# Kernel tuning notes

Hardware: AMD Instinct MI355X
Metric: run time of the kernel (lower is better)

Reference implementation:

```python
import jax, jax.numpy as jnp
import numpy as np

B = 65536      # batch
C = 1000       # num_classes
D = 256        # feat_dim


def _l2norm(x, eps=1e-12):
    # matches F.normalize(dim=1): v / max(||v||_2, eps)
    n = jnp.linalg.norm(x, axis=1, keepdims=True)
    return x / jnp.maximum(n, eps)


def setup_inputs() -> dict:
    key = jax.random.key(0)
    k1, k2, k3, k4, k5 = jax.random.split(key, 5)
    bound = 1.0 / np.sqrt(D)
    X = jax.random.normal(k1, (B, D), dtype=jnp.float32)
    labels = jax.random.randint(k2, (B,), 0, C)
    signatures = jax.random.uniform(k3, (C, D), dtype=jnp.float32, minval=-bound, maxval=bound)
    b_means = jax.random.uniform(k4, (1, D), dtype=jnp.float32, minval=-bound, maxval=bound)
    b_covs = jax.random.normal(k5, (D, D), dtype=jnp.float32)
    return {"X": X, "labels": labels, "signatures": signatures,
            "b_means": b_means, "b_covs": b_covs}


def reference(X, labels, signatures, b_means, b_covs):
    # SVD-based whitening of background covariance (tiny DxD)
    cov = b_covs @ b_covs.T
    U, eig, _ = jnp.linalg.svd(cov)
    DU = (eig ** -0.5)[:, None] * U.T              # diag(eig^-1/2) @ U^T, [D, D]
    xHat = _l2norm((X - b_means) @ DU.T)           # [B, D]
    sHat = _l2norm(signatures @ DU.T)              # [C, D]
    ACE_targets = xHat @ sHat.T                    # [B, C] cosine scores
    labels = labels.astype(jnp.int32)
    numerator = jnp.take_along_axis(ACE_targets, labels[:, None], axis=1)[:, 0]
    # denominator = exp(true) + sum(exp(others)) == sum over all classes
    loss = -jnp.mean(numerator - jax.nn.logsumexp(ACE_targets, axis=1))
    return (loss, ACE_targets)
```

## Files before the change

### kernel.cpp

```cpp
#include <hip/hip_runtime.h>
#include <hip/hip_bf16.h>
#include <math.h>

#define D_ 256
#define B_ 65536
#define C_ 1000

typedef _Float16 f16x8 __attribute__((ext_vector_type(8)));
typedef _Float16 f16x4 __attribute__((ext_vector_type(4)));
typedef float f32x4 __attribute__((ext_vector_type(4)));

__global__ void transpose_kernel(const float* __restrict__ in, float* __restrict__ out,
                                 double* __restrict__ acc) {
  __shared__ float t[32][33];
  if (blockIdx.x == 0 && threadIdx.x == 0) *acc = 0.0;
  const int bx = blockIdx.x & 7, by = blockIdx.x >> 3;
  const int lx = threadIdx.x & 31, ly = threadIdx.x >> 5;
#pragma unroll
  for (int s = 0; s < 4; ++s) {
    int r = by * 32 + ly + s * 8;
    t[ly + s * 8][lx] = in[r * 256 + bx * 32 + lx];
  }
  __syncthreads();
#pragma unroll
  for (int s = 0; s < 4; ++s) {
    int r = bx * 32 + ly + s * 8;
    out[r * 256 + by * 32 + lx] = t[lx][ly + s * 8];
  }
}

__global__ void cov_kernel(const float* __restrict__ bc, const float* __restrict__ bcT,
                           double* __restrict__ C64) {
  const int i = blockIdx.x, j = threadIdx.x;
  __shared__ float ri[D_];
  ri[j] = bc[i * D_ + j];
  __syncthreads();
  double s = 0.0;
#pragma unroll 8
  for (int k = 0; k < D_; ++k) s += (double)ri[k] * (double)bcT[k * D_ + j];
  C64[i * D_ + j] = s;
}

__global__ __launch_bounds__(256, 1) void chol_panel(double* __restrict__ A, int p) {
  const int j0 = p * 64;
  const int r = threadIdx.x;
  __shared__ double rowv[64];
  __shared__ double dinv;
  double pr[64];
  const bool act = (r >= j0);
  if (act) {
#pragma unroll
    for (int k = 0; k < 64; ++k) pr[k] = A[(size_t)r * D_ + j0 + k];
  }
#pragma unroll
  for (int j = 0; j < 64; ++j) {
    const int col = j0 + j;
    if (r == col) { double d = sqrt(pr[j]); pr[j] = d; dinv = 1.0 / d; }
    __syncthreads();
    if (r > col) {
      double lr = pr[j] * dinv;
      pr[j] = lr;
      if (r < j0 + 64) rowv[r - j0] = lr;
    }
    __syncthreads();
    if (r > col) {
      const double lr = pr[j];
#pragma unroll
      for (int k = j + 1; k < 64; ++k) pr[k] -= lr * rowv[k];
    }
  }
  if (act) {
    const int kmax = (r - j0 < 63) ? (r - j0) : 63;
#pragma unroll
    for (int k = 0; k < 64; ++k)
      if (k <= kmax) A[(size_t)r * D_ + j0 + k] = pr[k];
  }
}

__global__ __launch_bounds__(256) void chol_trail(double* __restrict__ A, int p) {
  const int j0 = p * 64;
  const int t0 = j0 + 64;
  int b = blockIdx.x, I = 0;
  while (b >= I + 1) { b -= I + 1; ++I; }
  const int J = b;
  const int r0 = t0 + I * 64, c0 = t0 + J * 64;
  __shared__ double LR[64][67];
  __shared__ double LC[64][67];
  const int tid = threadIdx.x;
  for (int e = tid; e < 64 * 64; e += 256) {
    int rr = e >> 6, cc = e & 63;
    LR[rr][cc] = A[(size_t)(r0 + rr) * D_ + j0 + cc];
    LC[rr][cc] = A[(size_t)(c0 + rr) * D_ + j0 + cc];
  }
  __syncthreads();
  const int tx = tid & 15, ty = tid >> 4;
  double acc[4][4];
#pragma unroll
  for (int i = 0; i < 4; ++i)
#pragma unroll
    for (int j = 0; j < 4; ++j) acc[i][j] = 0.0;
#pragma unroll 4
  for (int k = 0; k < 64; ++k) {
    double a_[4], b_[4];
#pragma unroll
    for (int i = 0; i < 4; ++i) a_[i] = LR[ty + 16 * i][k];
#pragma unroll
    for (int j = 0; j < 4; ++j) b_[j] = LC[tx + 16 * j][k];
#pragma unroll
    for (int i = 0; i < 4; ++i)
#pragma unroll
      for (int j = 0; j < 4; ++j) acc[i][j] += a_[i] * b_[j];
  }
#pragma unroll
  for (int i = 0; i < 4; ++i) {
    const int grow = r0 + ty + 16 * i;
#pragma unroll
    for (int j = 0; j < 4; ++j) {
      const int gcol = c0 + tx + 16 * j;
      A[(size_t)grow * D_ + gcol] -= acc[i][j];
    }
  }
}

__global__ __launch_bounds__(256) void inv_kernel(const double* __restrict__ L,
                                                  _Float16* __restrict__ Wb,
                                                  _Float16* __restrict__ WbT) {
  const int c = blockIdx.x;
  const int tid = threadIdx.x;
  __shared__ double w[D_];
  __shared__ double rdi[D_];
  __shared__ double rhs[32];
  __shared__ double Ldd[32][33];
  w[tid] = 0.0;
  rdi[tid] = 1.0 / L[(size_t)tid * D_ + tid];
  __syncthreads();
  const int q0 = c >> 5;
  for (int q = q0; q < 8; ++q) {
    const int i0 = q * 32;
    const int ii = tid >> 3, s = tid & 7;
    const int i = i0 + ii;
    double part = 0.0;
    for (int k = c + s; k < i0; k += 8) part += L[(size_t)i * D_ + k] * w[k];
    part += __shfl_xor(part, 1, 64);
    part += __shfl_xor(part, 2, 64);
    part += __shfl_xor(part, 4, 64);
    if (s == 0) rhs[ii] = ((i == c) ? 1.0 : 0.0) - part;
    for (int e = tid; e < 32 * 32; e += 256) {
      int rr = e >> 5, cc = e & 31;
      Ldd[rr][cc] = L[(size_t)(i0 + rr) * D_ + i0 + cc];
    }
    __syncthreads();
    if (tid < 32) {
      double x = rhs[tid];
      double v = 0.0;
      for (int j = 0; j < 32; ++j) {
        double xj = __shfl(x, j, 64);
        double wj = xj * rdi[i0 + j];
        if (tid == j) v = wj;
        if (tid > j) x -= Ldd[tid][j] * wj;
      }
      w[i0 + tid] = v;
    }
    __syncthreads();
  }
  _Float16 h = (_Float16)(float)w[tid];
  WbT[(size_t)c * D_ + tid] = h;
  Wb[(size_t)tid * D_ + c] = h;
}

__global__ void sig_kernel(const float* __restrict__ S, const _Float16* __restrict__ WbT,
                           _Float16* __restrict__ sHatP) {
  int c = blockIdx.x, i = threadIdx.x;
  const int g = c >> 4, lr = c & 15;
  const int ks = i >> 5, lq = (i >> 3) & 3, jj = i & 7;
  const size_t off = (size_t)(g * 8 + ks) * 512 + (size_t)(lq * 16 + lr) * 8 + jj;
  if (c >= C_) { sHatP[off] = (_Float16)0.0f; return; }
  __shared__ float srow[D_];
  __shared__ float wred[4];
  srow[i] = S[c * D_ + i];
  __syncthreads();
  float t = 0.f;
  for (int k = 0; k < D_; ++k) t += (float)WbT[k * D_ + i] * srow[k];
  float ss = t * t;
#pragma unroll
  for (int d = 1; d < 64; d <<= 1) ss += __shfl_xor(ss, d, 64);
  if ((i & 63) == 0) wred[i >> 6] = ss;
  __syncthreads();
  float tot = wred[0] + wred[1] + wred[2] + wred[3];
  float rn = 1.0f / fmaxf(sqrtf(tot), 1e-12f);
  sHatP[off] = (_Float16)(t * rn);
}

__global__ __launch_bounds__(256) void xform_kernel(const float* __restrict__ X,
                                                    const float* __restrict__ means,
                                                    const _Float16* __restrict__ Wb,
                                                    _Float16* __restrict__ xHat,
                                                    float* __restrict__ rnX) {
  __shared__ __align__(16) _Float16 As[64 * D_];
  __shared__ __align__(16) _Float16 Bs[128 * D_];
  __shared__ float msh[D_];
  const int tid = threadIdx.x;
  const int rowbase = blockIdx.x * 64;
  msh[tid] = means[tid];
  __syncthreads();
  for (int s = 0; s < 16; ++s) {
    int c = s * 256 + tid;
    int r = c >> 6, q = c & 63;
    const float4 xv = *(const float4*)(X + (size_t)(rowbase + r) * D_ + q * 4);
    f16x4 hv;
    hv[0] = (_Float16)(xv.x - msh[q * 4 + 0]);
    hv[1] = (_Float16)(xv.y - msh[q * 4 + 1]);
    hv[2] = (_Float16)(xv.z - msh[q * 4 + 2]);
    hv[3] = (_Float16)(xv.w - msh[q * 4 + 3]);
    int byte = (q * 8) ^ ((r & 7) << 4);
    *(f16x4*)((char*)(As + r * D_) + byte) = hv;
  }
  const int w = tid >> 6, l = tid & 63, lr = l & 15, lq = l >> 4;
  float ss[4] = {0.f, 0.f, 0.f, 0.f};
  for (int ch = 0; ch < 2; ++ch) {
    __syncthreads();
    for (int s = 0; s < 16; ++s) {
      int c = s * 256 + tid;
      int r = c >> 5, q = c & 31;
      uint4 v = *(const uint4*)(Wb + (size_t)(ch * 128 + r) * D_ + q * 8);
      int byte = (q * 16) ^ ((r & 7) << 4);
      *(uint4*)((char*)(Bs + r * D_) + byte) = v;
    }
    __syncthreads();
    f32x4 acc[8];
#pragma unroll
    for (int t = 0; t < 8; ++t) acc[t] = (f32x4){0.f, 0.f, 0.f, 0.f};
#pragma unroll
    for (int ks = 0; ks < 8; ++ks) {
      int arow = w * 16 + lr;
      int abyte = (ks * 64 + lq * 16) ^ ((arow & 7) << 4);
      f16x8 af = *(const f16x8*)((char*)(As + arow * D_) + abyte);
#pragma unroll
      for (int t = 0; t < 8; ++t) {
        int brow = t * 16 + lr;
        int bbyte = (ks * 64 + lq * 16) ^ ((brow & 7) << 4);
        f16x8 bf = *(const f16x8*)((char*)(Bs + brow * D_) + bbyte);
        acc[t] = __builtin_amdgcn_mfma_f32_16x16x32_f16(af, bf, acc[t], 0, 0, 0);
      }
    }
#pragma unroll
    for (int t = 0; t < 8; ++t) {
      int col = ch * 128 + t * 16 + lr;
#pragma unroll
      for (int j = 0; j < 4; ++j) {
        int row = rowbase + w * 16 + lq * 4 + j;
        float v = acc[t][j];
        ss[j] += v * v;
        xHat[(size_t)row * D_ + col] = (_Float16)v;
      }
    }
  }
#pragma unroll
  for (int d = 1; d < 16; d <<= 1) {
#pragma unroll
    for (int j = 0; j < 4; ++j) ss[j] += __shfl_xor(ss[j], d, 64);
  }
  if (lr == 0) {
#pragma unroll
    for (int j = 0; j < 4; ++j) {
      int row = rowbase + w * 16 + lq * 4 + j;
      rnX[row] = 1.0f / fmaxf(sqrtf(ss[j]), 1e-12f);
    }
  }
}

__global__ __launch_bounds__(512) void ace_kernel(const _Float16* __restrict__ xHat,
                                                  const _Float16* __restrict__ sHatP,
                                                  const float* __restrict__ rnX,
                                                  const int* __restrict__ labels,
                                                  float* __restrict__ outACE,
                                                  double* __restrict__ acc_loss) {
  __shared__ __align__(16) _Float16 Bsh[2][64 * 512];
  __shared__ float part[32];
  const int tid = threadIdx.x;
  const int wid = tid >> 6, l = tid & 63, lr = l & 15, lq = l >> 4;
  const int rowbase = blockIdx.x * 128;
  const int wrow = rowbase + wid * 16;

  f16x8 a[8];
  {
    const _Float16* ap = xHat + (size_t)(wrow + lr) * D_ + lq * 8;
#pragma unroll
    for (int ks = 0; ks < 8; ++ks) a[ks] = *(const f16x8*)(ap + ks * 32);
  }

  int lab[4]; float rx[4], ssum[4], num[4];
#pragma unroll
  for (int j = 0; j < 4; ++j) {
    int row = wrow + lq * 4 + j;
    lab[j] = labels[row];
    rx[j] = rnX[row];
    ssum[j] = 0.f; num[j] = 0.f;
  }

#define STAGE(bufi, chi) do {                                                        \
    const _Float16* _src = sHatP + (size_t)(chi) * 32768;                            \
    _Float16* _dst = &Bsh[bufi][0];                                                  \
    _Pragma("unroll")                                                                \
    for (int _s = 0; _s < 8; ++_s) {                                                 \
      const int _off = wid * 4096 + _s * 512;                                        \
      __builtin_amdgcn_global_load_lds(                                              \
          (const __attribute__((address_space(1))) unsigned int*)(_src + _off + l * 8), \
          (__attribute__((address_space(3))) unsigned int*)(_dst + _off), 16, 0, 0); \
    } } while (0)

  float* const outrow = outACE + (size_t)(wrow + lq * 4) * C_;

  STAGE(0, 0);
  __syncthreads();
  int buf = 0;
  for (int ch = 0; ch < 8; ++ch) {
    if (ch < 7) STAGE(buf ^ 1, ch + 1);
    const _Float16* bb = &Bsh[buf][(size_t)l * 8];
    f32x4 acc[8];
#pragma unroll
    for (int t = 0; t < 8; ++t) acc[t] = (f32x4){0.f, 0.f, 0.f, 0.f};
#pragma unroll
    for (int ks = 0; ks < 8; ++ks) {
#pragma unroll
      for (int t = 0; t < 8; ++t) {
        f16x8 bf = *(const f16x8*)(bb + (t * 8 + ks) * 512);
        acc[t] = __builtin_amdgcn_mfma_f32_16x16x32_f16(a[ks], bf, acc[t], 0, 0, 0);
      }
    }
#pragma unroll
    for (int t = 0; t < 8; ++t) {
      const int col = ch * 128 + t * 16 + lr;
      const bool valid = (col < C_);
#pragma unroll
      for (int j = 0; j < 4; ++j) {
        float v = acc[t][j] * rx[j];
        if (valid) outrow[(size_t)j * C_ + col] = v;
        ssum[j] += __expf(v - 1.0f);
        num[j] = (col == lab[j]) ? v : num[j];
      }
    }
    __syncthreads();
    buf ^= 1;
  }
#undef STAGE

#pragma unroll
  for (int d2 = 1; d2 < 16; d2 <<= 1) {
#pragma unroll
    for (int j = 0; j < 4; ++j) {
      ssum[j] += __shfl_xor(ssum[j], d2, 64);
      num[j]  += __shfl_xor(num[j], d2, 64);
    }
  }
  if (lr == 0 && lq == 0) {
  }
  if (lr == 0) {
    const float padcorr = 24.0f * __expf(-1.0f);
    float contrib = 0.f;
#pragma unroll
    for (int j = 0; j < 4; ++j)
      contrib += num[j] - (1.0f + __logf(ssum[j] - padcorr));
    part[wid * 4 + lq] = contrib;
  }
  __syncthreads();
  if (tid == 0) {
    float s = 0.f;
#pragma unroll
    for (int p2 = 0; p2 < 32; ++p2) s += part[p2];
    atomicAdd(acc_loss, (double)s);
  }
}

__global__ void fin_kernel(const double* a, float* out) {
  out[0] = (float)(-(*a) / (double)B_);
}

extern "C" void kernel_launch(void* const* d_in, const int* in_sizes, int n_in,
                              void* d_out, int out_size, void* d_ws, size_t ws_size,
                              hipStream_t stream) {
  const float* X      = (const float*)d_in[0];
  const int*   labels = (const int*)d_in[1];
  const float* S      = (const float*)d_in[2];
  const float* means  = (const float*)d_in[3];
  const float* bc     = (const float*)d_in[4];
  float* out = (float*)d_out;

  char* w = (char*)d_ws;
  double*    acc   = (double*)(w + 0);
  double*    C64   = (double*)(w + 256);
  _Float16*  Wb    = (_Float16*)(w + 524544);
  _Float16*  WbT   = (_Float16*)(w + 655616);
  _Float16*  sHatP = (_Float16*)(w + 786688);
  float*     rnX   = (float*)(w + 1310976);
  _Float16*  xHat  = (_Float16*)(w + 1573120);
  float*     bcT   = (float*)(w + 1573120);

  transpose_kernel<<<64, 256, 0, stream>>>(bc, bcT, acc);
  cov_kernel<<<256, 256, 0, stream>>>(bc, bcT, C64);
  for (int p = 0; p < 4; ++p) {
    chol_panel<<<1, 256, 0, stream>>>(C64, p);
    int nt = 3 - p;
    if (nt > 0) chol_trail<<<nt * (nt + 1) / 2, 256, 0, stream>>>(C64, p);
  }
  inv_kernel<<<256, 256, 0, stream>>>(C64, Wb, WbT);
  sig_kernel<<<1024, 256, 0, stream>>>(S, WbT, sHatP);
  xform_kernel<<<1024, 256, 0, stream>>>(X, means, Wb, xHat, rnX);
  ace_kernel<<<512, 512, 0, stream>>>(xHat, sHatP, rnX, labels, out + 1, acc);
  fin_kernel<<<1, 1, 0, stream>>>(acc, out);
}
```

Baseline: 388.3 us.

## Pre-pack whitening matrix for MFMA, stage it once per block, relax ace barriers

```diff
diff --git a/kernel.cpp b/kernel.cpp
--- a/kernel.cpp
+++ b/kernel.cpp
@@ -7,7 +7,6 @@
 #define C_ 1000
 
 typedef _Float16 f16x8 __attribute__((ext_vector_type(8)));
-typedef _Float16 f16x4 __attribute__((ext_vector_type(4)));
 typedef float f32x4 __attribute__((ext_vector_type(4)));
 
 __global__ void transpose_kernel(const float* __restrict__ in, float* __restrict__ out,
@@ -123,7 +122,7 @@
 }
 
 __global__ __launch_bounds__(256) void inv_kernel(const double* __restrict__ L,
-                                                  _Float16* __restrict__ Wb,
+                                                  _Float16* __restrict__ WbP,
                                                   _Float16* __restrict__ WbT) {
   const int c = blockIdx.x;
   const int tid = threadIdx.x;
@@ -165,7 +164,11 @@
   }
   _Float16 h = (_Float16)(float)w[tid];
   WbT[(size_t)c * D_ + tid] = h;
-  Wb[(size_t)tid * D_ + c] = h;
+  {
+    const int g = tid >> 4, lrr = tid & 15;
+    const int ks = c >> 5, lqq = (c >> 3) & 3, jj = c & 7;
+    WbP[(size_t)(g * 8 + ks) * 512 + (size_t)(lqq * 16 + lrr) * 8 + jj] = h;
+  }
 }
 
 __global__ void sig_kernel(const float* __restrict__ S, const _Float16* __restrict__ WbT,
@@ -191,64 +194,64 @@
   sHatP[off] = (_Float16)(t * rn);
 }
 
-__global__ __launch_bounds__(256) void xform_kernel(const float* __restrict__ X,
+__global__ __launch_bounds__(512) void xform_kernel(const float* __restrict__ X,
                                                     const float* __restrict__ means,
-                                                    const _Float16* __restrict__ Wb,
+                                                    const _Float16* __restrict__ WbP,
                                                     _Float16* __restrict__ xHat,
                                                     float* __restrict__ rnX) {
-  __shared__ __align__(16) _Float16 As[64 * D_];
-  __shared__ __align__(16) _Float16 Bs[128 * D_];
+  __shared__ __align__(16) _Float16 Wsh[65536];
   __shared__ float msh[D_];
   const int tid = threadIdx.x;
-  const int rowbase = blockIdx.x * 64;
-  msh[tid] = means[tid];
-  __syncthreads();
+  const int wid = tid >> 6, l = tid & 63, lr = l & 15, lq = l >> 4;
+  const int rowbase = blockIdx.x * 128;
+  const int arow = rowbase + wid * 16 + lr;
+  if (tid < 256) msh[tid] = means[tid];
+#pragma unroll
   for (int s = 0; s < 16; ++s) {
-    int c = s * 256 + tid;
-    int r = c >> 6, q = c & 63;
-    const float4 xv = *(const float4*)(X + (size_t)(rowbase + r) * D_ + q * 4);
-    f16x4 hv;
-    hv[0] = (_Float16)(xv.x - msh[q * 4 + 0]);
-    hv[1] = (_Float16)(xv.y - msh[q * 4 + 1]);
-    hv[2] = (_Float16)(xv.z - msh[q * 4 + 2]);
-    hv[3] = (_Float16)(xv.w - msh[q * 4 + 3]);
-    int byte = (q * 8) ^ ((r & 7) << 4);
-    *(f16x4*)((char*)(As + r * D_) + byte) = hv;
-  }
-  const int w = tid >> 6, l = tid & 63, lr = l & 15, lq = l >> 4;
+    const int off = (wid * 16 + s) * 512;
+    __builtin_amdgcn_global_load_lds(
+        (const __attribute__((address_space(1))) unsigned int*)(WbP + off + l * 8),
+        (__attribute__((address_space(3))) unsigned int*)(&Wsh[off]), 16, 0, 0);
+  }
+  __syncthreads();
+
+  f16x8 af[8];
+#pragma unroll
+  for (int ks = 0; ks < 8; ++ks) {
+    const float* xp = X + (size_t)arow * D_ + lq * 8 + ks * 32;
+    const float4 x0 = *(const float4*)(xp);
+    const float4 x1 = *(const float4*)(xp + 4);
+    const int mb = lq * 8 + ks * 32;
+    af[ks][0] = (_Float16)(x0.x - msh[mb + 0]);
+    af[ks][1] = (_Float16)(x0.y - msh[mb + 1]);
+    af[ks][2] = (_Float16)(x0.z - msh[mb + 2]);
+    af[ks][3] = (_Float16)(x0.w - msh[mb + 3]);
+    af[ks][4] = (_Float16)(x1.x - msh[mb + 4]);
+    af[ks][5] = (_Float16)(x1.y - msh[mb + 5]);
+    af[ks][6] = (_Float16)(x1.z - msh[mb + 6]);
+    af[ks][7] = (_Float16)(x1.w - msh[mb + 7]);
+  }
+
   float ss[4] = {0.f, 0.f, 0.f, 0.f};
+  const _Float16* bb = &Wsh[(size_t)l * 8];
   for (int ch = 0; ch < 2; ++ch) {
-    __syncthreads();
-    for (int s = 0; s < 16; ++s) {
-      int c = s * 256 + tid;
-      int r = c >> 5, q = c & 31;
-      uint4 v = *(const uint4*)(Wb + (size_t)(ch * 128 + r) * D_ + q * 8);
-      int byte = (q * 16) ^ ((r & 7) << 4);
-      *(uint4*)((char*)(Bs + r * D_) + byte) = v;
-    }
-    __syncthreads();
     f32x4 acc[8];
 #pragma unroll
     for (int t = 0; t < 8; ++t) acc[t] = (f32x4){0.f, 0.f, 0.f, 0.f};
 #pragma unroll
     for (int ks = 0; ks < 8; ++ks) {
-      int arow = w * 16 + lr;
-      int abyte = (ks * 64 + lq * 16) ^ ((arow & 7) << 4);
-      f16x8 af = *(const f16x8*)((char*)(As + arow * D_) + abyte);
 #pragma unroll
       for (int t = 0; t < 8; ++t) {
-        int brow = t * 16 + lr;
-        int bbyte = (ks * 64 + lq * 16) ^ ((brow & 7) << 4);
-        f16x8 bf = *(const f16x8*)((char*)(Bs + brow * D_) + bbyte);
-        acc[t] = __builtin_amdgcn_mfma_f32_16x16x32_f16(af, bf, acc[t], 0, 0, 0);
+        f16x8 bf = *(const f16x8*)(bb + (ch * 64 + t * 8 + ks) * 512);
+        acc[t] = __builtin_amdgcn_mfma_f32_16x16x32_f16(af[ks], bf, acc[t], 0, 0, 0);
       }
     }
 #pragma unroll
     for (int t = 0; t < 8; ++t) {
-      int col = ch * 128 + t * 16 + lr;
+      const int col = ch * 128 + t * 16 + lr;
 #pragma unroll
       for (int j = 0; j < 4; ++j) {
-        int row = rowbase + w * 16 + lq * 4 + j;
+        const int row = rowbase + wid * 16 + lq * 4 + j;
         float v = acc[t][j];
         ss[j] += v * v;
         xHat[(size_t)row * D_ + col] = (_Float16)v;
@@ -263,7 +266,7 @@
   if (lr == 0) {
 #pragma unroll
     for (int j = 0; j < 4; ++j) {
-      int row = rowbase + w * 16 + lq * 4 + j;
+      const int row = rowbase + wid * 16 + lq * 4 + j;
       rnX[row] = 1.0f / fmaxf(sqrtf(ss[j]), 1e-12f);
     }
   }
@@ -315,7 +318,10 @@
   __syncthreads();
   int buf = 0;
   for (int ch = 0; ch < 8; ++ch) {
-    if (ch < 7) STAGE(buf ^ 1, ch + 1);
+    if (ch < 7) {
+      STAGE(buf ^ 1, ch + 1);
+      __builtin_amdgcn_sched_barrier(0);
+    }
     const _Float16* bb = &Bsh[buf][(size_t)l * 8];
     f32x4 acc[8];
 #pragma unroll
@@ -340,7 +346,12 @@
         num[j] = (col == lab[j]) ? v : num[j];
       }
     }
-    __syncthreads();
+    if (ch < 7) {
+      __builtin_amdgcn_sched_barrier(0);
+      asm volatile("s_waitcnt vmcnt(32)" ::: "memory");
+      __builtin_amdgcn_s_barrier();
+      __builtin_amdgcn_sched_barrier(0);
+    }
     buf ^= 1;
   }
 #undef STAGE
@@ -352,8 +363,6 @@
       ssum[j] += __shfl_xor(ssum[j], d2, 64);
       num[j]  += __shfl_xor(num[j], d2, 64);
     }
-  }
-  if (lr == 0 && lq == 0) {
   }
   if (lr == 0) {
     const float padcorr = 24.0f * __expf(-1.0f);
@@ -389,7 +398,7 @@
   char* w = (char*)d_ws;
   double*    acc   = (double*)(w + 0);
   double*    C64   = (double*)(w + 256);
-  _Float16*  Wb    = (_Float16*)(w + 524544);
+  _Float16*  WbP   = (_Float16*)(w + 524544);
   _Float16*  WbT   = (_Float16*)(w + 655616);
   _Float16*  sHatP = (_Float16*)(w + 786688);
   float*     rnX   = (float*)(w + 1310976);
@@ -403,9 +412,9 @@
     int nt = 3 - p;
     if (nt > 0) chol_trail<<<nt * (nt + 1) / 2, 256, 0, stream>>>(C64, p);
   }
-  inv_kernel<<<256, 256, 0, stream>>>(C64, Wb, WbT);
+  inv_kernel<<<256, 256, 0, stream>>>(C64, WbP, WbT);
   sig_kernel<<<1024, 256, 0, stream>>>(S, WbT, sHatP);
-  xform_kernel<<<1024, 256, 0, stream>>>(X, means, Wb, xHat, rnX);
+  xform_kernel<<<512, 512, 0, stream>>>(X, means, WbP, xHat, rnX);
   ace_kernel<<<512, 512, 0, stream>>>(xHat, sHatP, rnX, labels, out + 1, acc);
   fin_kernel<<<1, 1, 0, stream>>>(acc, out);
 }
```

Result: faster. 372.0 us (-4.2%).
